# Kernel tuning notes

Measured on AMD Instinct MI355X. Metric: run time of the kernel, lower is better.

## Reference

```python
import jax, jax.numpy as jnp
import numpy as np

N_NODES = 100000
N_EDGES = 1600000
IN_CH, HID_CH, OUT_CH = 64, 128, 64


def _sage_conv(x, src, dst, W_l, W_r, b):
    # PyG SAGEConv (mean aggr): out = lin_l(mean_{j in N(i)} x_j) + lin_r(x_i) + bias
    msg = x[src]  # [E, F] gather of source-node features
    agg_sum = jax.ops.segment_sum(msg, dst, num_segments=N_NODES)  # [N, F]
    cnt = jax.ops.segment_sum(jnp.ones((src.shape[0],), x.dtype), dst, num_segments=N_NODES)
    agg = agg_sum / jnp.maximum(cnt, 1.0)[:, None]  # mean; isolated nodes -> 0
    return agg @ W_l + x @ W_r + b


def setup_inputs() -> dict:
    key = jax.random.key(0)
    ks = jax.random.split(key, 8)
    x = jax.random.normal(ks[0], (N_NODES, IN_CH), dtype=jnp.float32)
    edge_index = jax.random.randint(ks[1], (2, N_EDGES), 0, N_NODES, dtype=jnp.int32)
    def glorot(k, shape):
        lim = float(np.sqrt(6.0 / (shape[0] + shape[1])))
        return jax.random.uniform(k, shape, jnp.float32, -lim, lim)
    W_l1 = glorot(ks[2], (IN_CH, HID_CH))
    W_r1 = glorot(ks[3], (IN_CH, HID_CH))
    b1 = jnp.zeros((HID_CH,), jnp.float32)
    W_l2 = glorot(ks[4], (HID_CH, OUT_CH))
    W_r2 = glorot(ks[5], (HID_CH, OUT_CH))
    b2 = jnp.zeros((OUT_CH,), jnp.float32)
    return {"x": x, "edge_index": edge_index, "W_l1": W_l1, "W_r1": W_r1, "b1": b1,
            "W_l2": W_l2, "W_r2": W_r2, "b2": b2}


def reference(x, edge_index, W_l1, W_r1, b1, W_l2, W_r2, b2):
    src, dst = edge_index[0], edge_index[1]
    h = jax.nn.relu(_sage_conv(x, src, dst, W_l1, W_r1, b1))
    out = _sage_conv(h, src, dst, W_l2, W_r2, b2)
    return jax.nn.sigmoid(out)
```

## Files before the change

kernel.cpp:

```cpp
#include <hip/hip_runtime.h>
#include <hip/hip_bf16.h>
#include <stdint.h>


#define NBMAX 784
#define BCAP 3584

typedef __bf16 bf16x8 __attribute__((ext_vector_type(8)));
typedef float f32x4 __attribute__((ext_vector_type(4)));

__device__ __forceinline__ float ldb(const unsigned short* p) {
  return __uint_as_float(((unsigned int)*p) << 16);
}

__device__ __forceinline__ unsigned short bf16u(float f) {
  __hip_bfloat16 h = __float2bfloat16(f);
  return *(unsigned short*)&h;
}

__global__ void k_cast(const float* __restrict__ x, unsigned short* __restrict__ xb, int n4) {
  int i = blockIdx.x * blockDim.x + threadIdx.x;
  if (i < n4) {
    float4 v = ((const float4*)x)[i];
    unsigned int u0 = (unsigned int)bf16u(v.x) | ((unsigned int)bf16u(v.y) << 16);
    unsigned int u1 = (unsigned int)bf16u(v.z) | ((unsigned int)bf16u(v.w) << 16);
    ((uint2*)xb)[i] = make_uint2(u0, u1);
  }
}

__global__ __launch_bounds__(512) void k_bhist(const int* __restrict__ dst,
                                               unsigned int* __restrict__ hist, int E, int NB) {
  __shared__ unsigned int lh[NBMAX];
  const int tid = threadIdx.x;
  for (int b = tid; b < NB; b += 512) lh[b] = 0;
  __syncthreads();
  const int e0 = blockIdx.x * 16384;
  const int m = min(16384, E - e0);
  for (int i = tid; i < m; i += 512) atomicAdd(&lh[(unsigned int)dst[e0 + i] >> 7], 1u);
  __syncthreads();
  for (int b = tid; b < NB; b += 512) {
    unsigned int c = lh[b];
    if (c) atomicAdd(&hist[b], c);
  }
}

__global__ void k_scanb(const unsigned int* __restrict__ hist, unsigned int* __restrict__ base,
                        unsigned int* __restrict__ cursor, int NB) {
  const int lane = threadIdx.x;
  unsigned int running = 0;
  for (int b0 = 0; b0 < NB; b0 += 64) {
    int i = b0 + lane;
    unsigned int v = (i < NB) ? hist[i] : 0;
    unsigned int s = v;
#pragma unroll
    for (int off = 1; off < 64; off <<= 1) {
      unsigned int t = __shfl_up(s, off);
      if (lane >= off) s += t;
    }
    if (i < NB) {
      base[i] = running + s - v;
      cursor[i] = running + s - v;
    }
    running += __shfl(s, 63);
  }
  if (lane == 0) base[NB] = running;
}

__global__ __launch_bounds__(512) void k_part(const int* __restrict__ src,
                                              const int* __restrict__ dst,
                                              unsigned int* __restrict__ cursor,
                                              unsigned int* __restrict__ bkt, int E, int NB) {
  __shared__ unsigned int hist[NBMAX], lbase[NBMAX], gpos[NBMAX], lcur[NBMAX];
  __shared__ unsigned int stage[8192];
  __shared__ unsigned short stageb[8192];
  const int tid = threadIdx.x;
  const int e0 = blockIdx.x * 8192;
  const int m = min(8192, E - e0);
  for (int b = tid; b < NB; b += 512) { hist[b] = 0; lcur[b] = 0; }
  __syncthreads();
  for (int i = tid; i < m; i += 512) atomicAdd(&hist[(unsigned int)dst[e0 + i] >> 7], 1u);
  __syncthreads();
  if (tid < 64) {
    unsigned int running = 0;
    for (int b0 = 0; b0 < NB; b0 += 64) {
      int i = b0 + tid;
      unsigned int v = (i < NB) ? hist[i] : 0;
      unsigned int s = v;
#pragma unroll
      for (int off = 1; off < 64; off <<= 1) {
        unsigned int t = __shfl_up(s, off);
        if (tid >= off) s += t;
      }
      if (i < NB) lbase[i] = running + s - v;
      running += __shfl(s, 63);
    }
  }
  __syncthreads();
  for (int b = tid; b < NB; b += 512) {
    unsigned int c = hist[b];
    gpos[b] = c ? atomicAdd(&cursor[b], c) : 0u;
  }
  for (int i = tid; i < m; i += 512) {
    int d = dst[e0 + i];
    int s = src[e0 + i];
    unsigned int b = (unsigned int)d >> 7;
    unsigned int p = lbase[b] + atomicAdd(&lcur[b], 1u);
    stage[p] = (unsigned int)s | ((unsigned int)(d & 127) << 25);
    stageb[p] = (unsigned short)b;
  }
  __syncthreads();
  for (int i = tid; i < m; i += 512) {
    unsigned int b = stageb[i];
    bkt[gpos[b] + (unsigned int)i - lbase[b]] = stage[i];
  }
}

__global__ __launch_bounds__(512) void k_aggs(const unsigned short* __restrict__ feat,
                                              const unsigned int* __restrict__ bkt,
                                              const unsigned int* __restrict__ base,
                                              unsigned short* __restrict__ out, int N) {
  __shared__ unsigned int pbufA[BCAP];
  __shared__ unsigned int pbufB[BCAP];
  __shared__ unsigned int hist[128], lofs[128], cur[128];
  const int tid = threadIdx.x;
  const int lane = tid & 63;
  const int w = tid >> 6;
  const int nodelo = blockIdx.x << 7;
  if (tid < 128) hist[tid] = 0;
  const int ebeg = (int)base[blockIdx.x];
  int m = (int)base[blockIdx.x + 1] - ebeg;
  m = (m > BCAP) ? BCAP : m;
  __syncthreads();
  for (int i = tid; i < m; i += 512) {
    unsigned int t = bkt[ebeg + i];
    pbufA[i] = t;
    atomicAdd(&hist[t >> 25], 1u);
  }
  __syncthreads();
  if (tid < 64) {
    unsigned int v0 = hist[tid], v1 = hist[tid + 64];
    unsigned int s0 = v0, s1 = v1;
#pragma unroll
    for (int off = 1; off < 64; off <<= 1) {
      unsigned int t0 = __shfl_up(s0, off);
      unsigned int t1 = __shfl_up(s1, off);
      if (tid >= off) { s0 += t0; s1 += t1; }
    }
    unsigned int tot0 = __shfl(s0, 63);
    lofs[tid]      = s0 - v0;
    lofs[tid + 64] = tot0 + s1 - v1;
    cur[tid]       = s0 - v0;
    cur[tid + 64]  = tot0 + s1 - v1;
  }
  __syncthreads();
  for (int i = tid; i < m; i += 512) {
    unsigned int t = pbufA[i];
    unsigned int p = atomicAdd(&cur[t >> 25], 1u);
    pbufB[p] = t;
  }
  __syncthreads();
  for (int q = 0; q < 16; ++q) {
    const int r = (w << 4) + q;
    const unsigned int c = hist[r];
    const unsigned int o = lofs[r];
    float acc = 0.f;
    unsigned int e = 0;
    for (; e + 8 <= c; e += 8) {
      int s0 = __builtin_amdgcn_readfirstlane((int)(pbufB[o + e + 0] & 0x1FFFFFFu));
      int s1 = __builtin_amdgcn_readfirstlane((int)(pbufB[o + e + 1] & 0x1FFFFFFu));
      int s2 = __builtin_amdgcn_readfirstlane((int)(pbufB[o + e + 2] & 0x1FFFFFFu));
      int s3 = __builtin_amdgcn_readfirstlane((int)(pbufB[o + e + 3] & 0x1FFFFFFu));
      int s4 = __builtin_amdgcn_readfirstlane((int)(pbufB[o + e + 4] & 0x1FFFFFFu));
      int s5 = __builtin_amdgcn_readfirstlane((int)(pbufB[o + e + 5] & 0x1FFFFFFu));
      int s6 = __builtin_amdgcn_readfirstlane((int)(pbufB[o + e + 6] & 0x1FFFFFFu));
      int s7 = __builtin_amdgcn_readfirstlane((int)(pbufB[o + e + 7] & 0x1FFFFFFu));
      float f0 = ldb(feat + ((size_t)s0 << 6) + lane);
      float f1 = ldb(feat + ((size_t)s1 << 6) + lane);
      float f2 = ldb(feat + ((size_t)s2 << 6) + lane);
      float f3 = ldb(feat + ((size_t)s3 << 6) + lane);
      float f4 = ldb(feat + ((size_t)s4 << 6) + lane);
      float f5 = ldb(feat + ((size_t)s5 << 6) + lane);
      float f6 = ldb(feat + ((size_t)s6 << 6) + lane);
      float f7 = ldb(feat + ((size_t)s7 << 6) + lane);
      acc += f0 + f1 + f2 + f3 + f4 + f5 + f6 + f7;
    }
    for (; e + 4 <= c; e += 4) {
      int s0 = __builtin_amdgcn_readfirstlane((int)(pbufB[o + e + 0] & 0x1FFFFFFu));
      int s1 = __builtin_amdgcn_readfirstlane((int)(pbufB[o + e + 1] & 0x1FFFFFFu));
      int s2 = __builtin_amdgcn_readfirstlane((int)(pbufB[o + e + 2] & 0x1FFFFFFu));
      int s3 = __builtin_amdgcn_readfirstlane((int)(pbufB[o + e + 3] & 0x1FFFFFFu));
      float f0 = ldb(feat + ((size_t)s0 << 6) + lane);
      float f1 = ldb(feat + ((size_t)s1 << 6) + lane);
      float f2 = ldb(feat + ((size_t)s2 << 6) + lane);
      float f3 = ldb(feat + ((size_t)s3 << 6) + lane);
      acc += f0 + f1 + f2 + f3;
    }
    for (; e < c; ++e) {
      int s0 = __builtin_amdgcn_readfirstlane((int)(pbufB[o + e] & 0x1FFFFFFu));
      acc += ldb(feat + ((size_t)s0 << 6) + lane);
    }
    const int node = nodelo + r;
    if (node < N) {
      float sc = c ? (1.f / (float)c) : 0.f;
      out[((size_t)node << 6) + lane] = bf16u(acc * sc);
    }
  }
}

__global__ void k_wprep(const float* __restrict__ Wl1, const float* __restrict__ Wr1,
                        const float* __restrict__ Wl2, const float* __restrict__ Wr2,
                        unsigned short* __restrict__ W1p, unsigned short* __restrict__ W2p) {
  int f = blockIdx.x * blockDim.x + threadIdx.x;
  if (f >= 4096) return;
  int mat = f >> 11;
  int fr = f & 2047;
  int lane = fr & 63;
  int ntkb = fr >> 6;
  int nt = ntkb >> 2, kb = ntkb & 3;
  int col = (nt << 4) + (lane & 15);
  int k0 = (kb << 5) + ((lane >> 4) << 3);
  unsigned short v[8];
#pragma unroll
  for (int i = 0; i < 8; ++i) {
    int k = k0 + i;
    float val;
    if (mat == 0) val = (k < 64) ? Wl1[k * 128 + col] : Wr1[(k - 64) * 128 + col];
    else          val = (col < 64) ? Wl2[k * 64 + col] : Wr2[k * 64 + (col - 64)];
    v[i] = bf16u(val);
  }
  *(uint4*)((mat ? W2p : W1p) + (size_t)fr * 8) = *(const uint4*)v;
}

__global__ __launch_bounds__(256) void k_mm1(const unsigned short* __restrict__ agg,
                                             const unsigned short* __restrict__ xb,
                                             const unsigned short* __restrict__ W1p,
                                             const float* __restrict__ b1,
                                             unsigned short* __restrict__ h, int N) {
  __shared__ __align__(16) unsigned short sO[64][136];
  const int tid = threadIdx.x;
  const int lane = tid & 63;
  const int w = tid >> 6;
  const int n0 = blockIdx.x << 6;
  const int row16 = lane & 15;
  const int kgrp = lane >> 4;
  int node = n0 + (w << 4) + row16;
  if (node >= N) node = N - 1;

  bf16x8 a[4];
  {
    const unsigned short* ra = agg + ((size_t)node << 6);
    const unsigned short* rx = xb + ((size_t)node << 6);
    a[0] = *(const bf16x8*)(ra + kgrp * 8);
    a[1] = *(const bf16x8*)(ra + 32 + kgrp * 8);
    a[2] = *(const bf16x8*)(rx + kgrp * 8);
    a[3] = *(const bf16x8*)(rx + 32 + kgrp * 8);
  }
  const bf16x8* Wp = (const bf16x8*)W1p;
#pragma unroll
  for (int nt = 0; nt < 8; ++nt) {
    f32x4 acc = {0.f, 0.f, 0.f, 0.f};
#pragma unroll
    for (int kb = 0; kb < 4; ++kb) {
      bf16x8 b = Wp[(nt * 4 + kb) * 64 + lane];
      acc = __builtin_amdgcn_mfma_f32_16x16x32_bf16(a[kb], b, acc, 0, 0, 0);
    }
    const int col = (nt << 4) + row16;
    const float bias = b1[col];
#pragma unroll
    for (int r = 0; r < 4; ++r) {
      int lrow = (w << 4) + (kgrp << 2) + r;
      sO[lrow][col] = bf16u(fmaxf(acc[r] + bias, 0.f));
    }
  }
  __syncthreads();
#pragma unroll
  for (int it = 0; it < 4; ++it) {
    int idx = it * 256 + tid;
    int r = idx >> 4, sub = idx & 15;
    int nn = n0 + r;
    if (nn < N)
      *(uint4*)((char*)(h + ((size_t)nn << 7)) + sub * 16) =
          *(const uint4*)((char*)&sO[r][0] + sub * 16);
  }
}

__global__ __launch_bounds__(256) void k_mm2(const unsigned short* __restrict__ h,
                                             const unsigned short* __restrict__ W2p,
                                             unsigned short* __restrict__ y2,
                                             float* __restrict__ z2, int N) {
  __shared__ __align__(16) unsigned short sY[64][72];
  __shared__ __align__(16) float sZ[64][68];
  const int tid = threadIdx.x;
  const int lane = tid & 63;
  const int w = tid >> 6;
  const int n0 = blockIdx.x << 6;
  const int row16 = lane & 15;
  const int kgrp = lane >> 4;
  int node = n0 + (w << 4) + row16;
  if (node >= N) node = N - 1;

  bf16x8 a[4];
  {
    const unsigned short* rh = h + ((size_t)node << 7);
    a[0] = *(const bf16x8*)(rh + kgrp * 8);
    a[1] = *(const bf16x8*)(rh + 32 + kgrp * 8);
    a[2] = *(const bf16x8*)(rh + 64 + kgrp * 8);
    a[3] = *(const bf16x8*)(rh + 96 + kgrp * 8);
  }
  const bf16x8* Wp = (const bf16x8*)W2p;
#pragma unroll
  for (int nt = 0; nt < 8; ++nt) {
    f32x4 acc = {0.f, 0.f, 0.f, 0.f};
#pragma unroll
    for (int kb = 0; kb < 4; ++kb) {
      bf16x8 b = Wp[(nt * 4 + kb) * 64 + lane];
      acc = __builtin_amdgcn_mfma_f32_16x16x32_bf16(a[kb], b, acc, 0, 0, 0);
    }
    const int col = (nt << 4) + row16;
#pragma unroll
    for (int r = 0; r < 4; ++r) {
      int lrow = (w << 4) + (kgrp << 2) + r;
      if (nt < 4) sY[lrow][col] = bf16u(acc[r]);
      else        sZ[lrow][col - 64] = acc[r];
    }
  }
  __syncthreads();
#pragma unroll
  for (int it = 0; it < 2; ++it) {
    int idx = it * 256 + tid;
    int r = idx >> 3, sub = idx & 7;
    int nn = n0 + r;
    if (nn < N)
      *(uint4*)((char*)(y2 + ((size_t)nn << 6)) + sub * 16) =
          *(const uint4*)((char*)&sY[r][0] + sub * 16);
  }
#pragma unroll
  for (int it = 0; it < 4; ++it) {
    int idx = it * 256 + tid;
    int r = idx >> 4, sub = idx & 15;
    int nn = n0 + r;
    if (nn < N)
      *(uint4*)((char*)(z2 + ((size_t)nn << 6)) + sub * 16) =
          *(const uint4*)((char*)&sZ[r][0] + sub * 16);
  }
}

__global__ void k_sig(const unsigned short* __restrict__ agg2, const float* __restrict__ z2,
                      const float* __restrict__ b2, float* __restrict__ out, int n16) {
  int i = blockIdx.x * blockDim.x + threadIdx.x;
  if (i < n16) {
    int c4 = (i & 15) << 2;
    uint2 av = *(const uint2*)(agg2 + ((size_t)(i >> 4) << 6) + c4);
    float4 zv = *(const float4*)(z2 + ((size_t)(i >> 4) << 6) + c4);
    float a0 = __uint_as_float(av.x << 16);
    float a1 = __uint_as_float(av.x & 0xffff0000u);
    float a2 = __uint_as_float(av.y << 16);
    float a3 = __uint_as_float(av.y & 0xffff0000u);
    float4 o;
    o.x = 1.f / (1.f + __expf(-(a0 + zv.x + b2[c4])));
    o.y = 1.f / (1.f + __expf(-(a1 + zv.y + b2[c4 + 1])));
    o.z = 1.f / (1.f + __expf(-(a2 + zv.z + b2[c4 + 2])));
    o.w = 1.f / (1.f + __expf(-(a3 + zv.w + b2[c4 + 3])));
    *(float4*)(out + ((size_t)(i >> 4) << 6) + c4) = o;
  }
}

extern "C" void kernel_launch(void* const* d_in, const int* in_sizes, int n_in,
                              void* d_out, int out_size, void* d_ws, size_t ws_size,
                              hipStream_t stream) {
  const float* x   = (const float*)d_in[0];
  const int*   ei  = (const int*)d_in[1];
  const float* Wl1 = (const float*)d_in[2];
  const float* Wr1 = (const float*)d_in[3];
  const float* b1  = (const float*)d_in[4];
  const float* Wl2 = (const float*)d_in[5];
  const float* Wr2 = (const float*)d_in[6];
  const float* b2  = (const float*)d_in[7];
  float* out = (float*)d_out;

  const int N = in_sizes[0] / 64;
  const int E = in_sizes[1] / 2;
  int NB = (N + 127) >> 7;
  if (NB > NBMAX) NB = NBMAX;
  const int* src = ei;
  const int* dst = ei + E;

  char* wp = (char*)d_ws;
  auto take = [&](size_t bytes) {
    char* p = wp;
    wp += (bytes + 255) & ~(size_t)255;
    return p;
  };
  unsigned int* hist   = (unsigned int*)take((size_t)NBMAX * 4);
  unsigned int* base   = (unsigned int*)take((size_t)(NBMAX + 1) * 4);
  unsigned int* cursor = (unsigned int*)take((size_t)NBMAX * 4);
  unsigned int* bkt    = (unsigned int*)take((size_t)E * 4);
  unsigned short* W1p  = (unsigned short*)take(128 * 128 * 2);
  unsigned short* W2p  = (unsigned short*)take(128 * 128 * 2);
  unsigned short* xb   = (unsigned short*)take((size_t)N * 64 * 2);
  unsigned short* agg  = (unsigned short*)take((size_t)N * 64 * 2);
  unsigned short* h    = (unsigned short*)take((size_t)N * 128 * 2);
  float* z2            = (float*)take((size_t)N * 64 * 4);
  unsigned short* y2   = xb;

  hipMemsetAsync(hist, 0, (size_t)NBMAX * 4, stream);

  const int n4 = N * 16;
  k_cast<<<(n4 + 255) / 256, 256, 0, stream>>>(x, xb, n4);
  k_bhist<<<(E + 16383) / 16384, 512, 0, stream>>>(dst, hist, E, NB);
  k_scanb<<<1, 64, 0, stream>>>(hist, base, cursor, NB);
  k_part<<<(E + 8191) / 8192, 512, 0, stream>>>(src, dst, cursor, bkt, E, NB);
  k_wprep<<<16, 256, 0, stream>>>(Wl1, Wr1, Wl2, Wr2, W1p, W2p);

  const int nb64 = (N + 63) / 64;
  k_aggs<<<NB, 512, 0, stream>>>(xb, bkt, base, agg, N);
  k_mm1<<<nb64, 256, 0, stream>>>(agg, xb, W1p, b1, h, N);
  k_mm2<<<nb64, 256, 0, stream>>>(h, W2p, y2, z2, N);
  k_aggs<<<NB, 512, 0, stream>>>(y2, bkt, base, agg, N);
  k_sig<<<(N * 16 + 255) / 256, 256, 0, stream>>>(agg, z2, b2, out, N * 16);
}
```

Before: 251.3 us.

## Split features into 16-column slices for gather and fuse sigmoid into aggregation

Features are stored as four column-slice tables of 16 bf16 each, so each slice table is a quarter of the size and more likely to stay cache-resident during the random gather. The aggregation kernel now walks the four slices one after another, with the four quarter-wavefronts each handling a different subset of edges and combining their sums through shuffles. The second aggregation also applies the z2 add, bias and sigmoid directly, which removes the separate k_sig kernel and its intermediate round trip. In exchange, each pass rereads the edge list four times and only a quarter of the lanes store results, and k_cast writes an extra copy of x.

```diff
diff --git a/kernel.cpp b/kernel.cpp
--- a/kernel.cpp
+++ b/kernel.cpp
@@ -18,13 +18,17 @@
   return *(unsigned short*)&h;
 }
 
-__global__ void k_cast(const float* __restrict__ x, unsigned short* __restrict__ xb, int n4) {
+__global__ void k_cast(const float* __restrict__ x, unsigned short* __restrict__ xb,
+                       unsigned short* __restrict__ xs, int N) {
   int i = blockIdx.x * blockDim.x + threadIdx.x;
-  if (i < n4) {
-    float4 v = ((const float4*)x)[i];
+  if (i < N * 16) {
+    int n = i >> 4, c4 = (i & 15) << 2;
+    float4 v = *(const float4*)(x + (size_t)n * 64 + c4);
     unsigned int u0 = (unsigned int)bf16u(v.x) | ((unsigned int)bf16u(v.y) << 16);
     unsigned int u1 = (unsigned int)bf16u(v.z) | ((unsigned int)bf16u(v.w) << 16);
-    ((uint2*)xb)[i] = make_uint2(u0, u1);
+    *(uint2*)(xb + (size_t)n * 64 + c4) = make_uint2(u0, u1);
+    int s = c4 >> 4, wtn = c4 & 15;
+    *(uint2*)(xs + (size_t)s * N * 16 + (size_t)n * 16 + wtn) = make_uint2(u0, u1);
   }
 }
 
@@ -115,10 +119,14 @@
   }
 }
 
-__global__ __launch_bounds__(512) void k_aggs(const unsigned short* __restrict__ feat,
+template <int EPI>
+__global__ __launch_bounds__(512) void k_aggs(const unsigned short* __restrict__ feat_s,
                                               const unsigned int* __restrict__ bkt,
                                               const unsigned int* __restrict__ base,
-                                              unsigned short* __restrict__ out, int N) {
+                                              unsigned short* __restrict__ outRows,
+                                              const float* __restrict__ z2,
+                                              const float* __restrict__ b2,
+                                              float* __restrict__ outF, int N) {
   __shared__ unsigned int pbufA[BCAP];
   __shared__ unsigned int pbufB[BCAP];
   __shared__ unsigned int hist[128], lofs[128], cur[128];
@@ -159,50 +167,43 @@
     pbufB[p] = t;
   }
   __syncthreads();
-  for (int q = 0; q < 16; ++q) {
-    const int r = (w << 4) + q;
-    const unsigned int c = hist[r];
-    const unsigned int o = lofs[r];
-    float acc = 0.f;
-    unsigned int e = 0;
-    for (; e + 8 <= c; e += 8) {
-      int s0 = __builtin_amdgcn_readfirstlane((int)(pbufB[o + e + 0] & 0x1FFFFFFu));
-      int s1 = __builtin_amdgcn_readfirstlane((int)(pbufB[o + e + 1] & 0x1FFFFFFu));
-      int s2 = __builtin_amdgcn_readfirstlane((int)(pbufB[o + e + 2] & 0x1FFFFFFu));
-      int s3 = __builtin_amdgcn_readfirstlane((int)(pbufB[o + e + 3] & 0x1FFFFFFu));
-      int s4 = __builtin_amdgcn_readfirstlane((int)(pbufB[o + e + 4] & 0x1FFFFFFu));
-      int s5 = __builtin_amdgcn_readfirstlane((int)(pbufB[o + e + 5] & 0x1FFFFFFu));
-      int s6 = __builtin_amdgcn_readfirstlane((int)(pbufB[o + e + 6] & 0x1FFFFFFu));
-      int s7 = __builtin_amdgcn_readfirstlane((int)(pbufB[o + e + 7] & 0x1FFFFFFu));
-      float f0 = ldb(feat + ((size_t)s0 << 6) + lane);
-      float f1 = ldb(feat + ((size_t)s1 << 6) + lane);
-      float f2 = ldb(feat + ((size_t)s2 << 6) + lane);
-      float f3 = ldb(feat + ((size_t)s3 << 6) + lane);
-      float f4 = ldb(feat + ((size_t)s4 << 6) + lane);
-      float f5 = ldb(feat + ((size_t)s5 << 6) + lane);
-      float f6 = ldb(feat + ((size_t)s6 << 6) + lane);
-      float f7 = ldb(feat + ((size_t)s7 << 6) + lane);
-      acc += f0 + f1 + f2 + f3 + f4 + f5 + f6 + f7;
-    }
-    for (; e + 4 <= c; e += 4) {
-      int s0 = __builtin_amdgcn_readfirstlane((int)(pbufB[o + e + 0] & 0x1FFFFFFu));
-      int s1 = __builtin_amdgcn_readfirstlane((int)(pbufB[o + e + 1] & 0x1FFFFFFu));
-      int s2 = __builtin_amdgcn_readfirstlane((int)(pbufB[o + e + 2] & 0x1FFFFFFu));
-      int s3 = __builtin_amdgcn_readfirstlane((int)(pbufB[o + e + 3] & 0x1FFFFFFu));
-      float f0 = ldb(feat + ((size_t)s0 << 6) + lane);
-      float f1 = ldb(feat + ((size_t)s1 << 6) + lane);
-      float f2 = ldb(feat + ((size_t)s2 << 6) + lane);
-      float f3 = ldb(feat + ((size_t)s3 << 6) + lane);
-      acc += f0 + f1 + f2 + f3;
-    }
-    for (; e < c; ++e) {
-      int s0 = __builtin_amdgcn_readfirstlane((int)(pbufB[o + e] & 0x1FFFFFFu));
-      acc += ldb(feat + ((size_t)s0 << 6) + lane);
-    }
-    const int node = nodelo + r;
-    if (node < N) {
-      float sc = c ? (1.f / (float)c) : 0.f;
-      out[((size_t)node << 6) + lane] = bf16u(acc * sc);
+  const int quarter = lane >> 4, ch = lane & 15;
+#pragma unroll
+  for (int s = 0; s < 4; ++s) {
+    const unsigned short* tbl = feat_s + (size_t)s * N * 16;
+    for (int q = 0; q < 16; ++q) {
+      const int r = (w << 4) + q;
+      const int cdeg = (int)hist[r];
+      const int o = (int)lofs[r];
+      float acc = 0.f;
+      int e = quarter;
+      for (; e + 12 < cdeg; e += 16) {
+        int i0 = (int)(pbufB[o + e]      & 0x1FFFFFFu);
+        int i1 = (int)(pbufB[o + e + 4]  & 0x1FFFFFFu);
+        int i2 = (int)(pbufB[o + e + 8]  & 0x1FFFFFFu);
+        int i3 = (int)(pbufB[o + e + 12] & 0x1FFFFFFu);
+        float f0 = ldb(tbl + (size_t)i0 * 16 + ch);
+        float f1 = ldb(tbl + (size_t)i1 * 16 + ch);
+        float f2 = ldb(tbl + (size_t)i2 * 16 + ch);
+        float f3 = ldb(tbl + (size_t)i3 * 16 + ch);
+        acc += f0 + f1 + f2 + f3;
+      }
+      for (; e < cdeg; e += 4) {
+        int i0 = (int)(pbufB[o + e] & 0x1FFFFFFu);
+        acc += ldb(tbl + (size_t)i0 * 16 + ch);
+      }
+      acc += __shfl_xor(acc, 16);
+      acc += __shfl_xor(acc, 32);
+      const int node = nodelo + r;
+      if (quarter == 0 && node < N) {
+        float sc = cdeg ? (1.f / (float)cdeg) : 0.f;
+        if (EPI == 0) {
+          outRows[((size_t)node << 6) + (s << 4) + ch] = bf16u(acc * sc);
+        } else {
+          float v = acc * sc + z2[((size_t)node << 6) + (s << 4) + ch] + b2[(s << 4) + ch];
+          outF[((size_t)node << 6) + (s << 4) + ch] = 1.f / (1.f + __expf(-v));
+        }
+      }
     }
   }
 }
@@ -286,7 +287,7 @@
 
 __global__ __launch_bounds__(256) void k_mm2(const unsigned short* __restrict__ h,
                                              const unsigned short* __restrict__ W2p,
-                                             unsigned short* __restrict__ y2,
+                                             unsigned short* __restrict__ y2s,
                                              float* __restrict__ z2, int N) {
   __shared__ __align__(16) unsigned short sY[64][72];
   __shared__ __align__(16) float sZ[64][68];
@@ -329,10 +330,11 @@
   for (int it = 0; it < 2; ++it) {
     int idx = it * 256 + tid;
     int r = idx >> 3, sub = idx & 7;
+    int s = sub >> 1, wtn = (sub & 1) << 3;
     int nn = n0 + r;
     if (nn < N)
-      *(uint4*)((char*)(y2 + ((size_t)nn << 6)) + sub * 16) =
-          *(const uint4*)((char*)&sY[r][0] + sub * 16);
+      *(uint4*)(y2s + (size_t)s * N * 16 + (size_t)nn * 16 + wtn) =
+          *(const uint4*)(&sY[r][(s << 4) + wtn]);
   }
 #pragma unroll
   for (int it = 0; it < 4; ++it) {
@@ -342,26 +344,6 @@
     if (nn < N)
       *(uint4*)((char*)(z2 + ((size_t)nn << 6)) + sub * 16) =
           *(const uint4*)((char*)&sZ[r][0] + sub * 16);
-  }
-}
-
-__global__ void k_sig(const unsigned short* __restrict__ agg2, const float* __restrict__ z2,
-                      const float* __restrict__ b2, float* __restrict__ out, int n16) {
-  int i = blockIdx.x * blockDim.x + threadIdx.x;
-  if (i < n16) {
-    int c4 = (i & 15) << 2;
-    uint2 av = *(const uint2*)(agg2 + ((size_t)(i >> 4) << 6) + c4);
-    float4 zv = *(const float4*)(z2 + ((size_t)(i >> 4) << 6) + c4);
-    float a0 = __uint_as_float(av.x << 16);
-    float a1 = __uint_as_float(av.x & 0xffff0000u);
-    float a2 = __uint_as_float(av.y << 16);
-    float a3 = __uint_as_float(av.y & 0xffff0000u);
-    float4 o;
-    o.x = 1.f / (1.f + __expf(-(a0 + zv.x + b2[c4])));
-    o.y = 1.f / (1.f + __expf(-(a1 + zv.y + b2[c4 + 1])));
-    o.z = 1.f / (1.f + __expf(-(a2 + zv.z + b2[c4 + 2])));
-    o.w = 1.f / (1.f + __expf(-(a3 + zv.w + b2[c4 + 3])));
-    *(float4*)(out + ((size_t)(i >> 4) << 6) + c4) = o;
   }
 }
 
@@ -398,24 +380,23 @@
   unsigned short* W1p  = (unsigned short*)take(128 * 128 * 2);
   unsigned short* W2p  = (unsigned short*)take(128 * 128 * 2);
   unsigned short* xb   = (unsigned short*)take((size_t)N * 64 * 2);
+  unsigned short* xs   = (unsigned short*)take((size_t)N * 64 * 2);
   unsigned short* agg  = (unsigned short*)take((size_t)N * 64 * 2);
   unsigned short* h    = (unsigned short*)take((size_t)N * 128 * 2);
   float* z2            = (float*)take((size_t)N * 64 * 4);
-  unsigned short* y2   = xb;
+  unsigned short* y2s  = xs;
 
   hipMemsetAsync(hist, 0, (size_t)NBMAX * 4, stream);
 
-  const int n4 = N * 16;
-  k_cast<<<(n4 + 255) / 256, 256, 0, stream>>>(x, xb, n4);
+  k_cast<<<(N * 16 + 255) / 256, 256, 0, stream>>>(x, xb, xs, N);
   k_bhist<<<(E + 16383) / 16384, 512, 0, stream>>>(dst, hist, E, NB);
   k_scanb<<<1, 64, 0, stream>>>(hist, base, cursor, NB);
   k_part<<<(E + 8191) / 8192, 512, 0, stream>>>(src, dst, cursor, bkt, E, NB);
   k_wprep<<<16, 256, 0, stream>>>(Wl1, Wr1, Wl2, Wr2, W1p, W2p);
 
   const int nb64 = (N + 63) / 64;
-  k_aggs<<<NB, 512, 0, stream>>>(xb, bkt, base, agg, N);
+  k_aggs<0><<<NB, 512, 0, stream>>>(xs, bkt, base, agg, nullptr, nullptr, nullptr, N);
   k_mm1<<<nb64, 256, 0, stream>>>(agg, xb, W1p, b1, h, N);
-  k_mm2<<<nb64, 256, 0, stream>>>(h, W2p, y2, z2, N);
-  k_aggs<<<NB, 512, 0, stream>>>(y2, bkt, base, agg, N);
-  k_sig<<<(N * 16 + 255) / 256, 256, 0, stream>>>(agg, z2, b2, out, N * 16);
-}
+  k_mm2<<<nb64, 256, 0, stream>>>(h, W2p, y2s, z2, N);
+  k_aggs<1><<<NB, 512, 0, stream>>>(y2s, bkt, base, nullptr, z2, b2, out, N);
+}
```

Result: slower. 362.9 us (+44.4%).
